# Optimization experiments

Hardware: AMD Instinct MI355X
Metric: run time of the kernel (lower is better)

Reference implementation:

```python
import jax, jax.numpy as jnp
import numpy as np
from jax.scipy.special import gammaln

TEMP = 1.0
PRIOR = 0.2
THRESHOLD = 0.5
EPS = 1e-12


def _normalize(x):
    # F.normalize: x / max(||x||_2, eps)
    n = jnp.linalg.norm(x, axis=-1, keepdims=True)
    return x / jnp.maximum(n, EPS)


def setup_inputs() -> dict:
    key = jax.random.key(0)
    k1, k2 = jax.random.split(key, 2)
    B, L, D = 8, 4096, 512
    hidden = jax.random.normal(k1, (B, L, D), dtype=jnp.float32)
    # uniform noise for RelaxedBernoulli rsample (probs shape is (B, L) after left-pad)
    noise = jax.random.uniform(k2, (B, L), dtype=jnp.float32, minval=1e-6, maxval=1.0 - 1e-6)
    # learned projections, initialized to identity as in the module
    q_w = jnp.eye(D, dtype=jnp.float32)
    k_w = jnp.eye(D, dtype=jnp.float32)
    return {"hidden": hidden, "q_w": q_w, "k_w": k_w, "noise": noise}


def reference(hidden, q_w, k_w, noise):
    B, L, D = hidden.shape
    # cosine-similarity boundary scoring between adjacent tokens
    q = _normalize(hidden[:, :-1]) @ q_w.T  # (B, L-1, D)
    k = _normalize(hidden[:, 1:]) @ k_w.T   # (B, L-1, D)
    cos_sim = jnp.einsum('bld,bld->bl', q, k)  # (B, L-1)
    probs = jnp.clip((1.0 - cos_sim) / 2.0, 0.0, 1.0)
    probs = jnp.pad(probs, ((0, 0), (1, 0)), constant_values=1.0)  # (B, L), first pos always boundary

    # RelaxedBernoulli rsample: sigmoid((logits + logistic_noise) / temp)
    logits = jnp.log(probs) - jnp.log1p(-probs)
    lnoise = jnp.log(noise) - jnp.log1p(-noise)
    soft_boundaries = jax.nn.sigmoid((logits + lnoise) / TEMP)

    # straight-through hard threshold
    hard_f = (soft_boundaries > THRESHOLD).astype(soft_boundaries.dtype)
    hard_boundaries = hard_f - jax.lax.stop_gradient(soft_boundaries) + soft_boundaries

    # dynamic segment pooling (`delete`): segment id = cumsum(boundaries) - 1,
    # mean-pool tokens of each segment; output padded to L segments.
    seg = jnp.clip(jnp.cumsum(hard_boundaries, axis=1).astype(jnp.int32) - 1, 0, L - 1)  # (B, L)

    def pool_one(h, s):
        sums = jax.ops.segment_sum(h, s, num_segments=L)                       # (L, D)
        cnts = jax.ops.segment_sum(jnp.ones((h.shape[0],), h.dtype), s, num_segments=L)
        return sums / jnp.maximum(cnts, 1.0)[:, None]

    pooled = jax.vmap(pool_one)(hidden, seg)   # (B, L, D) (empty segments are zeros)
    pooled = pooled.transpose(1, 0, 2)          # (L, B, D) per `.transpose(0, 1)`

    # Binomial(n=L, p=prior) log-prob loss on number of boundaries per row
    n = jnp.asarray(L, dtype=hidden.dtype)
    ksum = hard_boundaries.sum(axis=-1)  # (B,)
    log_prob = (gammaln(n + 1.0) - gammaln(ksum + 1.0) - gammaln(n - ksum + 1.0)
                + ksum * jnp.log(jnp.asarray(PRIOR, hidden.dtype))
                + (n - ksum) * jnp.log1p(-jnp.asarray(PRIOR, hidden.dtype)))
    loss = -jnp.mean(log_prob) / n
    return pooled, loss
```

## Files before the change

### kernel.cpp

```cpp
#include <hip/hip_runtime.h>
#include <hip/hip_bf16.h>
#include <math.h>

#define B_ 8
#define L_ 4096
#define D_ 512
#define STRIP 8

typedef float f4 __attribute__((ext_vector_type(4)));


__device__ __forceinline__ float wave_reduce_add(float v) {
#pragma unroll
    for (int o = 32; o > 0; o >>= 1) v += __shfl_xor(v, o, 64);
    return v;
}

__global__ __launch_bounds__(256) void k_check(const float* __restrict__ q_w,
                                               const float* __restrict__ k_w,
                                               int* __restrict__ nonid_arr) {
    int t = blockIdx.x * 256 + threadIdx.x;
    bool bad = false;
    for (int i4 = t; i4 < (D_ * D_) / 4; i4 += 64 * 256) {
        int flat = i4 * 4;
        int r = flat >> 9, c0 = flat & (D_ - 1);
        f4 q = *(const f4*)(q_w + flat);
        f4 k = *(const f4*)(k_w + flat);
        float ev[4] = {0.f, 0.f, 0.f, 0.f};
        int dj = r - c0;
        if (dj >= 0 && dj < 4) ev[dj] = 1.0f;
        bad |= (q.x != ev[0]) || (q.y != ev[1]) || (q.z != ev[2]) || (q.w != ev[3]);
        bad |= (k.x != ev[0]) || (k.y != ev[1]) || (k.z != ev[2]) || (k.w != ev[3]);
    }
    unsigned long long m = __ballot(bad);
    __shared__ unsigned long long s[4];
    if ((threadIdx.x & 63) == 0) s[threadIdx.x >> 6] = m;
    __syncthreads();
    if (threadIdx.x == 0)
        nonid_arr[blockIdx.x] = ((s[0] | s[1] | s[2] | s[3]) != 0ull) ? 1 : 0;
}

__global__ __launch_bounds__(256, 4) void k_dotdec(const float* __restrict__ hidden,
                                                   const float* __restrict__ noise,
                                                   const float* __restrict__ q_w,
                                                   const float* __restrict__ k_w,
                                                   const int* __restrict__ nonid_arr,
                                                   unsigned long long* __restrict__ hard64) {
    __shared__ float lds[4 * 2 * D_];
    int wid = threadIdx.x >> 6;
    int lane = threadIdx.x & 63;
    int wave = blockIdx.x * 4 + wid;
    int b = wave >> 9;
    int t0 = (wave & 511) * STRIP;
    const float* base = hidden + (size_t)b * L_ * D_;
    bool nonid = __any(nonid_arr[lane] != 0);
    int i0 = lane * 4, i1 = lane * 4 + 256;
    int rp = (t0 > 0) ? (t0 - 1) : 0;

    if (!nonid) {
        f4 A[9], Bv[9];
#pragma unroll
        for (int i = 0; i < 9; ++i) {
            int r = (i == 0) ? rp : (t0 + i - 1);
            const float* rc = base + (size_t)r * D_;
            A[i] = *(const f4*)(rc + i0);
            Bv[i] = *(const f4*)(rc + i1);
        }
        float ss0 = (A[0].x * A[0].x + A[0].y * A[0].y + A[0].z * A[0].z + A[0].w * A[0].w) +
                    (Bv[0].x * Bv[0].x + Bv[0].y * Bv[0].y + Bv[0].z * Bv[0].z + Bv[0].w * Bv[0].w);
        float dp[STRIP], sp[STRIP];
#pragma unroll
        for (int i = 0; i < STRIP; ++i) {
            dp[i] = (A[i].x * A[i + 1].x + A[i].y * A[i + 1].y +
                     A[i].z * A[i + 1].z + A[i].w * A[i + 1].w) +
                    (Bv[i].x * Bv[i + 1].x + Bv[i].y * Bv[i + 1].y +
                     Bv[i].z * Bv[i + 1].z + Bv[i].w * Bv[i + 1].w);
            sp[i] = (A[i + 1].x * A[i + 1].x + A[i + 1].y * A[i + 1].y +
                     A[i + 1].z * A[i + 1].z + A[i + 1].w * A[i + 1].w) +
                    (Bv[i + 1].x * Bv[i + 1].x + Bv[i + 1].y * Bv[i + 1].y +
                     Bv[i + 1].z * Bv[i + 1].z + Bv[i + 1].w * Bv[i + 1].w);
        }
        float ss0r = wave_reduce_add(ss0);
#pragma unroll
        for (int i = 0; i < STRIP; ++i) {
            dp[i] = wave_reduce_add(dp[i]);
            sp[i] = wave_reduce_add(sp[i]);
        }
        float myDp = dp[7], mySsr = sp[7], mySsl = sp[6];
#pragma unroll
        for (int i = 0; i < 7; ++i) {
            if (lane == i) {
                myDp = dp[i];
                mySsr = sp[i];
                mySsl = (i == 0) ? ss0r : sp[i - 1];
            }
        }
        float u = noise[b * L_ + t0 + (lane & 7)];
        float nl = fmaxf(sqrtf(mySsl), 1e-12f);
        float nr = fmaxf(sqrtf(mySsr), 1e-12f);
        float cosv = myDp / (nl * nr);
        float p = fminf(fmaxf(0.5f * (1.0f - cosv), 0.0f), 1.0f);
        float x = (logf(p) - log1pf(-p)) + (logf(u) - log1pf(-u));
        float sg = 1.0f / (1.0f + expf(-x));
        unsigned long long bm = __ballot(sg > 0.5f);
        if (lane == 0) {
            unsigned long long m = 0;
#pragma unroll
            for (int i = 0; i < 8; ++i) m |= ((bm >> i) & 1ull) << (8 * i);
            if (t0 == 0) m = (m & ~0xFFull) | 1ull;
            hard64[wave] = m;
        }
    } else {
        f4 pa = *(const f4*)(base + (size_t)rp * D_ + i0);
        f4 pb = *(const f4*)(base + (size_t)rp * D_ + i1);
        float ssl;
        {
            float s = pa.x * pa.x + pa.y * pa.y + pa.z * pa.z + pa.w * pa.w;
            float s2 = pb.x * pb.x + pb.y * pb.y + pb.z * pb.z + pb.w * pb.w;
            ssl = wave_reduce_add(s + s2);
        }
        unsigned long long mask = 0;
        for (int i = 0; i < STRIP; ++i) {
            int l = t0 + i;
            unsigned char h;
            const float* rc = base + (size_t)l * D_;
            f4 ca = *(const f4*)(rc + i0);
            f4 cb = *(const f4*)(rc + i1);
            float ssr = (ca.x * ca.x + ca.y * ca.y + ca.z * ca.z + ca.w * ca.w) +
                        (cb.x * cb.x + cb.y * cb.y + cb.z * cb.z + cb.w * cb.w);
            ssr = wave_reduce_add(ssr);
            if (l == 0) {
                h = 1;
            } else {
                float nl = fmaxf(sqrtf(ssl), 1e-12f);
                float nr = fmaxf(sqrtf(ssr), 1e-12f);
                float* nL = lds + wid * 2 * D_;
                float* nR = nL + D_;
                nL[i0 + 0] = pa.x / nl; nL[i0 + 1] = pa.y / nl;
                nL[i0 + 2] = pa.z / nl; nL[i0 + 3] = pa.w / nl;
                nL[i1 + 0] = pb.x / nl; nL[i1 + 1] = pb.y / nl;
                nL[i1 + 2] = pb.z / nl; nL[i1 + 3] = pb.w / nl;
                nR[i0 + 0] = ca.x / nr; nR[i0 + 1] = ca.y / nr;
                nR[i0 + 2] = ca.z / nr; nR[i0 + 3] = ca.w / nr;
                nR[i1 + 0] = cb.x / nr; nR[i1 + 1] = cb.y / nr;
                nR[i1 + 2] = cb.z / nr; nR[i1 + 3] = cb.w / nr;
                float acc = 0.f;
                for (int r8 = 0; r8 < 8; ++r8) {
                    int row = lane + 64 * r8;
                    float qi = 0.f, ki = 0.f;
                    for (int j = 0; j < D_; ++j) {
                        qi += q_w[row * D_ + j] * nL[j];
                        ki += k_w[row * D_ + j] * nR[j];
                    }
                    acc += qi * ki;
                }
                float cosv = wave_reduce_add(acc);
                float p = fminf(fmaxf(0.5f * (1.0f - cosv), 0.0f), 1.0f);
                float u = noise[b * L_ + l];
                float x = (logf(p) - log1pf(-p)) + (logf(u) - log1pf(-u));
                float sg = 1.0f / (1.0f + expf(-x));
                h = (sg > 0.5f) ? (unsigned char)1 : (unsigned char)0;
            }
            mask |= ((unsigned long long)h) << (8 * i);
            pa = ca; pb = cb; ssl = ssr;
        }
        if (lane == 0) hard64[wave] = mask;
    }
}

__global__ __launch_bounds__(256) void k_scan(const unsigned char* __restrict__ hard,
                                              int* __restrict__ seg_starts,
                                              int* __restrict__ ksum) {
    int b = blockIdx.x;
    int tid = threadIdx.x;
    int lane = tid & 63, w = tid >> 6;
    const uint4* hb = (const uint4*)(hard + b * L_);
    uint4 v = hb[tid];
    int s = __popc(v.x) + __popc(v.y) + __popc(v.z) + __popc(v.w);
    int incl = s;
#pragma unroll
    for (int off = 1; off < 64; off <<= 1) {
        int t = __shfl_up(incl, off, 64);
        if (lane >= off) incl += t;
    }
    __shared__ int wtot[4];
    if (lane == 63) wtot[w] = incl;
    __syncthreads();
    int woff = 0;
#pragma unroll
    for (int k = 0; k < 4; ++k)
        if (k < w) woff += wtot[k];
    int run = woff + incl - s;
    int base = tid * 16;
    unsigned wds[4] = {v.x, v.y, v.z, v.w};
#pragma unroll
    for (int wi = 0; wi < 4; ++wi)
#pragma unroll
        for (int byte = 0; byte < 4; ++byte)
            if ((wds[wi] >> (8 * byte)) & 1) {
                run++;
                seg_starts[b * L_ + run - 1] = base + wi * 4 + byte;
            }
    if (tid == 255) ksum[b] = woff + incl;
}

__global__ __launch_bounds__(256) void k_pool(const float* __restrict__ hidden,
                                              const int* __restrict__ seg_starts,
                                              const int* __restrict__ ksum,
                                              float* __restrict__ out,
                                              float* __restrict__ out_loss) {
    int wid = threadIdx.x >> 6, lane = threadIdx.x & 63;
    int j = blockIdx.x * 4 + wid, b = blockIdx.y;
    int S = ksum[b];
    int i0 = lane * 4, i1 = i0 + 256;
    f4 a0 = (f4)(0.0f);
    f4 a1 = (f4)(0.0f);
    if (j < S) {
        int start = seg_starts[b * L_ + j];
        int end = (j + 1 < S) ? seg_starts[b * L_ + j + 1] : L_;
        const float* base = hidden + ((size_t)b * L_ + start) * D_;
        for (int t = start; t < end; ++t, base += D_) {
            f4 v0 = *(const f4*)(base + i0);
            f4 v1 = *(const f4*)(base + i1);
            a0 += v0;
            a1 += v1;
        }
        float len = (float)(end - start);
        a0.x /= len; a0.y /= len; a0.z /= len; a0.w /= len;
        a1.x /= len; a1.y /= len; a1.z /= len; a1.w /= len;
    }
    float* o = out + ((size_t)j * B_ + b) * D_;
    __builtin_nontemporal_store(a0, (f4*)(o + i0));
    __builtin_nontemporal_store(a1, (f4*)(o + i1));

    if (blockIdx.x == gridDim.x - 1 && blockIdx.y == 0) {
        __shared__ double sh[17];
        int tid = threadIdx.x;
        double n = (double)L_;
        if (tid < 8) sh[tid] = lgamma((double)ksum[tid] + 1.0);
        else if (tid < 16) sh[tid] = lgamma(n - (double)ksum[tid - 8] + 1.0);
        else if (tid == 16) sh[16] = lgamma(n + 1.0);
        __syncthreads();
        if (tid == 0) {
            double acc = 0.0, lg = sh[16];
            for (int bb = 0; bb < 8; ++bb) {
                double k = (double)ksum[bb];
                acc += lg - sh[bb] - sh[8 + bb] + k * log(0.2) + (n - k) * log(0.8);
            }
            out_loss[0] = (float)(-(acc / 8.0) / n);
        }
    }
}

extern "C" void kernel_launch(void* const* d_in, const int* in_sizes, int n_in,
                              void* d_out, int out_size, void* d_ws, size_t ws_size,
                              hipStream_t stream) {
    const float* hidden = (const float*)d_in[0];
    const float* q_w = (const float*)d_in[1];
    const float* k_w = (const float*)d_in[2];
    const float* noise = (const float*)d_in[3];
    float* out = (float*)d_out;

    char* ws = (char*)d_ws;
    int* nonid_arr = (int*)(ws + 0);
    int* ksum = (int*)(ws + 512);
    unsigned char* hard = (unsigned char*)(ws + 1024);
    unsigned long long* hard64 = (unsigned long long*)(ws + 1024);
    int* seg_starts = (int*)(ws + 34816);

    k_check<<<64, 256, 0, stream>>>(q_w, k_w, nonid_arr);
    k_dotdec<<<(B_ * L_ / STRIP) / 4, 256, 0, stream>>>(hidden, noise, q_w, k_w,
                                                        nonid_arr, hard64);
    k_scan<<<B_, 256, 0, stream>>>(hard, seg_starts, ksum);
    k_pool<<<dim3(L_ / 4, B_), 256, 0, stream>>>(hidden, seg_starts, ksum, out,
                                                 out + (size_t)L_ * B_ * D_);
}
```

Before: 49.39 us.

## Fuse check, boundary, scan and pool stages into one cooperative persistent kernel

Merges the four separate launches into a single cooperative kernel that uses grid-wide syncs between the identity check, boundary decision, per-batch scan and segment pooling stages. Work is distributed with persistent grid-stride loops over waves, and pooling now processes 8 segments per wave. The aim is to remove inter-kernel launch gaps and tail effects. The cost is grid-sync overhead, and the scan stage runs on only 8 blocks while the rest of the grid waits. A fallback to the multi-kernel path is kept if the cooperative launch fails.

```diff
diff --git a/kernel.cpp b/kernel.cpp
--- a/kernel.cpp
+++ b/kernel.cpp
@@ -1,4 +1,5 @@
 #include <hip/hip_runtime.h>
+#include <hip/hip_cooperative_groups.h>
 #include <hip/hip_bf16.h>
 #include <math.h>
 
@@ -6,8 +7,12 @@
 #define L_ 4096
 #define D_ 512
 #define STRIP 8
+#define GRID_WANT 1024
+#define NWAVE (B_ * L_ / STRIP)
 
 typedef float f4 __attribute__((ext_vector_type(4)));
+
+namespace cg = cooperative_groups;
 
 
 __device__ __forceinline__ float wave_reduce_add(float v) {
@@ -16,44 +21,16 @@
     return v;
 }
 
-__global__ __launch_bounds__(256) void k_check(const float* __restrict__ q_w,
-                                               const float* __restrict__ k_w,
-                                               int* __restrict__ nonid_arr) {
-    int t = blockIdx.x * 256 + threadIdx.x;
-    bool bad = false;
-    for (int i4 = t; i4 < (D_ * D_) / 4; i4 += 64 * 256) {
-        int flat = i4 * 4;
-        int r = flat >> 9, c0 = flat & (D_ - 1);
-        f4 q = *(const f4*)(q_w + flat);
-        f4 k = *(const f4*)(k_w + flat);
-        float ev[4] = {0.f, 0.f, 0.f, 0.f};
-        int dj = r - c0;
-        if (dj >= 0 && dj < 4) ev[dj] = 1.0f;
-        bad |= (q.x != ev[0]) || (q.y != ev[1]) || (q.z != ev[2]) || (q.w != ev[3]);
-        bad |= (k.x != ev[0]) || (k.y != ev[1]) || (k.z != ev[2]) || (k.w != ev[3]);
-    }
-    unsigned long long m = __ballot(bad);
-    __shared__ unsigned long long s[4];
-    if ((threadIdx.x & 63) == 0) s[threadIdx.x >> 6] = m;
-    __syncthreads();
-    if (threadIdx.x == 0)
-        nonid_arr[blockIdx.x] = ((s[0] | s[1] | s[2] | s[3]) != 0ull) ? 1 : 0;
-}
-
-__global__ __launch_bounds__(256, 4) void k_dotdec(const float* __restrict__ hidden,
-                                                   const float* __restrict__ noise,
-                                                   const float* __restrict__ q_w,
-                                                   const float* __restrict__ k_w,
-                                                   const int* __restrict__ nonid_arr,
-                                                   unsigned long long* __restrict__ hard64) {
-    __shared__ float lds[4 * 2 * D_];
-    int wid = threadIdx.x >> 6;
-    int lane = threadIdx.x & 63;
-    int wave = blockIdx.x * 4 + wid;
+
+__device__ __forceinline__ void boundary_wave(int wave, const float* __restrict__ hidden,
+                                              const float* __restrict__ noise,
+                                              const float* __restrict__ q_w,
+                                              const float* __restrict__ k_w,
+                                              bool nonid, float* lds_wave, int lane,
+                                              unsigned long long* hard64) {
     int b = wave >> 9;
     int t0 = (wave & 511) * STRIP;
     const float* base = hidden + (size_t)b * L_ * D_;
-    bool nonid = __any(nonid_arr[lane] != 0);
     int i0 = lane * 4, i1 = lane * 4 + 256;
     int rp = (t0 > 0) ? (t0 - 1) : 0;
 
@@ -134,7 +111,7 @@
             } else {
                 float nl = fmaxf(sqrtf(ssl), 1e-12f);
                 float nr = fmaxf(sqrtf(ssr), 1e-12f);
-                float* nL = lds + wid * 2 * D_;
+                float* nL = lds_wave;
                 float* nR = nL + D_;
                 nL[i0 + 0] = pa.x / nl; nL[i0 + 1] = pa.y / nl;
                 nL[i0 + 2] = pa.z / nl; nL[i0 + 3] = pa.w / nl;
@@ -168,6 +145,174 @@
     }
 }
 
+__device__ __forceinline__ void pool_wave(int wave, const float* __restrict__ hidden,
+                                          const int* __restrict__ seg_starts,
+                                          const int* __restrict__ ksum, int lane,
+                                          float* __restrict__ out) {
+    int b = wave & 7;
+    int jbase = (wave >> 3) * 8;
+    int S = ksum[b];
+    int i0 = lane * 4, i1 = i0 + 256;
+    for (int k = 0; k < 8; ++k) {
+        int j = jbase + k;
+        f4 a0 = (f4)(0.0f);
+        f4 a1 = (f4)(0.0f);
+        if (j < S) {
+            int start = seg_starts[b * L_ + j];
+            int end = (j + 1 < S) ? seg_starts[b * L_ + j + 1] : L_;
+            const float* base = hidden + ((size_t)b * L_ + start) * D_;
+            for (int t = start; t < end; ++t, base += D_) {
+                a0 += *(const f4*)(base + i0);
+                a1 += *(const f4*)(base + i1);
+            }
+            float len = (float)(end - start);
+            a0.x /= len; a0.y /= len; a0.z /= len; a0.w /= len;
+            a1.x /= len; a1.y /= len; a1.z /= len; a1.w /= len;
+        }
+        float* o = out + ((size_t)j * B_ + b) * D_;
+        __builtin_nontemporal_store(a0, (f4*)(o + i0));
+        __builtin_nontemporal_store(a1, (f4*)(o + i1));
+    }
+}
+
+__global__ __launch_bounds__(256, 4) void k_fused(
+    const float* __restrict__ hidden, const float* __restrict__ noise,
+    const float* __restrict__ q_w, const float* __restrict__ k_w,
+    int* __restrict__ nonid_arr, int* __restrict__ ksum,
+    unsigned long long* hard64_arg,
+    int* __restrict__ seg_starts, float* __restrict__ out,
+    float* __restrict__ out_loss) {
+    cg::grid_group grid = cg::this_grid();
+    unsigned long long* hard64 = hard64_arg;
+    const unsigned char* hard = (const unsigned char*)hard64_arg;
+    int bid = blockIdx.x, tid = threadIdx.x;
+    int wid = tid >> 6, lane = tid & 63;
+    int nb = gridDim.x;
+
+    __shared__ float lds[4 * 2 * D_];
+    __shared__ unsigned long long sb[4];
+    __shared__ int wtot[4];
+    __shared__ double sh[17];
+
+    for (int c = bid; c < 256; c += nb) {
+        int flat = (c * 256 + tid) * 4;
+        int r = flat >> 9, c0 = flat & (D_ - 1);
+        f4 q = *(const f4*)(q_w + flat);
+        f4 k = *(const f4*)(k_w + flat);
+        float ev[4] = {0.f, 0.f, 0.f, 0.f};
+        int dj = r - c0;
+        if (dj >= 0 && dj < 4) ev[dj] = 1.0f;
+        bool bad = (q.x != ev[0]) || (q.y != ev[1]) || (q.z != ev[2]) || (q.w != ev[3]) ||
+                   (k.x != ev[0]) || (k.y != ev[1]) || (k.z != ev[2]) || (k.w != ev[3]);
+        unsigned long long m = __ballot(bad);
+        if (lane == 0) sb[wid] = m;
+        __syncthreads();
+        if (tid == 0)
+            nonid_arr[c] = ((sb[0] | sb[1] | sb[2] | sb[3]) != 0ull) ? 1 : 0;
+        __syncthreads();
+    }
+    grid.sync();
+
+    {
+        int4 nf = ((const int4*)nonid_arr)[lane];
+        bool nonid = __any((nf.x | nf.y | nf.z | nf.w) != 0);
+        for (int wave = bid * 4 + wid; wave < NWAVE; wave += nb * 4)
+            boundary_wave(wave, hidden, noise, q_w, k_w, nonid,
+                          lds + wid * 2 * D_, lane, hard64);
+    }
+    grid.sync();
+
+    if (bid < B_) {
+        int b = bid;
+        const uint4* hb = (const uint4*)(hard + b * L_);
+        uint4 v = hb[tid];
+        int s = __popc(v.x) + __popc(v.y) + __popc(v.z) + __popc(v.w);
+        int incl = s;
+#pragma unroll
+        for (int off = 1; off < 64; off <<= 1) {
+            int t = __shfl_up(incl, off, 64);
+            if (lane >= off) incl += t;
+        }
+        if (lane == 63) wtot[wid] = incl;
+        __syncthreads();
+        int woff = 0;
+#pragma unroll
+        for (int k = 0; k < 4; ++k)
+            if (k < wid) woff += wtot[k];
+        int run = woff + incl - s;
+        int base = tid * 16;
+        unsigned wds[4] = {v.x, v.y, v.z, v.w};
+#pragma unroll
+        for (int wi = 0; wi < 4; ++wi)
+#pragma unroll
+            for (int byte = 0; byte < 4; ++byte)
+                if ((wds[wi] >> (8 * byte)) & 1) {
+                    run++;
+                    seg_starts[b * L_ + run - 1] = base + wi * 4 + byte;
+                }
+        if (tid == 255) ksum[b] = woff + incl;
+    }
+    grid.sync();
+
+    for (int wave = bid * 4 + wid; wave < NWAVE; wave += nb * 4)
+        pool_wave(wave, hidden, seg_starts, ksum, lane, out);
+
+    if (bid == 0) {
+        double n = (double)L_;
+        if (tid < 8) sh[tid] = lgamma((double)ksum[tid] + 1.0);
+        else if (tid < 16) sh[tid] = lgamma(n - (double)ksum[tid - 8] + 1.0);
+        else if (tid == 16) sh[16] = lgamma(n + 1.0);
+        __syncthreads();
+        if (tid == 0) {
+            double acc = 0.0, lg = sh[16];
+            for (int bb = 0; bb < 8; ++bb) {
+                double k = (double)ksum[bb];
+                acc += lg - sh[bb] - sh[8 + bb] + k * log(0.2) + (n - k) * log(0.8);
+            }
+            out_loss[0] = (float)(-(acc / 8.0) / n);
+        }
+    }
+}
+
+__global__ __launch_bounds__(256) void k_check(const float* __restrict__ q_w,
+                                               const float* __restrict__ k_w,
+                                               int* __restrict__ nonid_arr) {
+    int t = blockIdx.x * 256 + threadIdx.x;
+    bool bad = false;
+    for (int i4 = t; i4 < (D_ * D_) / 4; i4 += 64 * 256) {
+        int flat = i4 * 4;
+        int r = flat >> 9, c0 = flat & (D_ - 1);
+        f4 q = *(const f4*)(q_w + flat);
+        f4 k = *(const f4*)(k_w + flat);
+        float ev[4] = {0.f, 0.f, 0.f, 0.f};
+        int dj = r - c0;
+        if (dj >= 0 && dj < 4) ev[dj] = 1.0f;
+        bad |= (q.x != ev[0]) || (q.y != ev[1]) || (q.z != ev[2]) || (q.w != ev[3]);
+        bad |= (k.x != ev[0]) || (k.y != ev[1]) || (k.z != ev[2]) || (k.w != ev[3]);
+    }
+    unsigned long long m = __ballot(bad);
+    __shared__ unsigned long long s[4];
+    if ((threadIdx.x & 63) == 0) s[threadIdx.x >> 6] = m;
+    __syncthreads();
+    if (threadIdx.x == 0)
+        nonid_arr[blockIdx.x] = ((s[0] | s[1] | s[2] | s[3]) != 0ull) ? 1 : 0;
+}
+
+__global__ __launch_bounds__(256, 4) void k_dotdec(const float* __restrict__ hidden,
+                                                   const float* __restrict__ noise,
+                                                   const float* __restrict__ q_w,
+                                                   const float* __restrict__ k_w,
+                                                   const int* __restrict__ nonid_arr,
+                                                   unsigned long long* __restrict__ hard64) {
+    __shared__ float lds[4 * 2 * D_];
+    int wid = threadIdx.x >> 6;
+    int lane = threadIdx.x & 63;
+    int wave = blockIdx.x * 4 + wid;
+    bool nonid = __any(nonid_arr[lane] != 0);
+    boundary_wave(wave, hidden, noise, q_w, k_w, nonid, lds + wid * 2 * D_, lane,
+                  hard64);
+}
+
 __global__ __launch_bounds__(256) void k_scan(const unsigned char* __restrict__ hard,
                                               int* __restrict__ seg_starts,
                                               int* __restrict__ ksum) {
@@ -210,30 +355,10 @@
                                               float* __restrict__ out,
                                               float* __restrict__ out_loss) {
     int wid = threadIdx.x >> 6, lane = threadIdx.x & 63;
-    int j = blockIdx.x * 4 + wid, b = blockIdx.y;
-    int S = ksum[b];
-    int i0 = lane * 4, i1 = i0 + 256;
-    f4 a0 = (f4)(0.0f);
-    f4 a1 = (f4)(0.0f);
-    if (j < S) {
-        int start = seg_starts[b * L_ + j];
-        int end = (j + 1 < S) ? seg_starts[b * L_ + j + 1] : L_;
-        const float* base = hidden + ((size_t)b * L_ + start) * D_;
-        for (int t = start; t < end; ++t, base += D_) {
-            f4 v0 = *(const f4*)(base + i0);
-            f4 v1 = *(const f4*)(base + i1);
-            a0 += v0;
-            a1 += v1;
-        }
-        float len = (float)(end - start);
-        a0.x /= len; a0.y /= len; a0.z /= len; a0.w /= len;
-        a1.x /= len; a1.y /= len; a1.z /= len; a1.w /= len;
-    }
-    float* o = out + ((size_t)j * B_ + b) * D_;
-    __builtin_nontemporal_store(a0, (f4*)(o + i0));
-    __builtin_nontemporal_store(a1, (f4*)(o + i1));
-
-    if (blockIdx.x == gridDim.x - 1 && blockIdx.y == 0) {
+    int wave = blockIdx.x * 4 + wid;
+    pool_wave(wave, hidden, seg_starts, ksum, lane, out);
+
+    if (blockIdx.x == gridDim.x - 1) {
         __shared__ double sh[17];
         int tid = threadIdx.x;
         double n = (double)L_;
@@ -260,18 +385,38 @@
     const float* k_w = (const float*)d_in[2];
     const float* noise = (const float*)d_in[3];
     float* out = (float*)d_out;
+    float* out_loss = out + (size_t)L_ * B_ * D_;
 
     char* ws = (char*)d_ws;
     int* nonid_arr = (int*)(ws + 0);
-    int* ksum = (int*)(ws + 512);
-    unsigned char* hard = (unsigned char*)(ws + 1024);
-    unsigned long long* hard64 = (unsigned long long*)(ws + 1024);
+    int* ksum = (int*)(ws + 1024);
+    unsigned char* hard = (unsigned char*)(ws + 2048);
+    unsigned long long* hard64 = (unsigned long long*)(ws + 2048);
     int* seg_starts = (int*)(ws + 34816);
 
-    k_check<<<64, 256, 0, stream>>>(q_w, k_w, nonid_arr);
-    k_dotdec<<<(B_ * L_ / STRIP) / 4, 256, 0, stream>>>(hidden, noise, q_w, k_w,
-                                                        nonid_arr, hard64);
-    k_scan<<<B_, 256, 0, stream>>>(hard, seg_starts, ksum);
-    k_pool<<<dim3(L_ / 4, B_), 256, 0, stream>>>(hidden, seg_starts, ksum, out,
-                                                 out + (size_t)L_ * B_ * D_);
-}
+    int numCU = 0, maxPerCU = 0;
+    int dev = 0;
+    bool coop_ok = (hipGetDevice(&dev) == hipSuccess) &&
+                   (hipDeviceGetAttribute(&numCU, hipDeviceAttributeMultiprocessorCount,
+                                          dev) == hipSuccess) &&
+                   (hipOccupancyMaxActiveBlocksPerMultiprocessor(&maxPerCU, k_fused, 256,
+                                                                 0) == hipSuccess) &&
+                   (maxPerCU >= 1) && (numCU * maxPerCU >= 8);
+    if (coop_ok) {
+        int G = numCU * maxPerCU;
+        if (G > GRID_WANT) G = GRID_WANT;
+        void* args[] = {(void*)&hidden, (void*)&noise, (void*)&q_w, (void*)&k_w,
+                        (void*)&nonid_arr, (void*)&ksum, (void*)&hard64,
+                        (void*)&seg_starts, (void*)&out, (void*)&out_loss};
+        coop_ok = (hipLaunchCooperativeKernel((void*)k_fused, dim3(G), dim3(256), args,
+                                              0, stream) == hipSuccess);
+    }
+    if (!coop_ok) {
+        k_check<<<64, 256, 0, stream>>>(q_w, k_w, nonid_arr);
+        k_dotdec<<<NWAVE / 4, 256, 0, stream>>>(hidden, noise, q_w, k_w, nonid_arr,
+                                                hard64);
+        k_scan<<<B_, 256, 0, stream>>>(hard, seg_starts, ksum);
+        k_pool<<<NWAVE / 4 / 8, 256, 0, stream>>>(hidden, seg_starts, ksum, out,
+                                                  out_loss);
+    }
+}
```

Result: slower. 189.8 us (+284.2%).

## Fuse identity check into dot kernel, split fixup path, merge scan with pooling

Applied to the files above, without the earlier changes.

Moves the q_w/k_w identity check into the main adjacency-dot kernel, so each of the 1024 blocks checks 256 weight elements. The general projection path moves to a separate fixup kernel that exits early when the weights are identity. The scan and pooling kernels merge into one: each block recomputes the row's segment starts into LDS and pools 32 segments, and the loss block recomputes per-row boundary counts. This cuts kernel launches and global seg_starts traffic, at the cost of a redundant scan in every pooling block and an extra fixup launch.

```diff
diff --git a/kernel.cpp b/kernel.cpp
--- a/kernel.cpp
+++ b/kernel.cpp
@@ -6,6 +6,7 @@
 #define L_ 4096
 #define D_ 512
 #define STRIP 8
+#define NWAVE (B_ * L_ / STRIP)
 
 typedef float f4 __attribute__((ext_vector_type(4)));
 
@@ -16,166 +17,184 @@
     return v;
 }
 
-__global__ __launch_bounds__(256) void k_check(const float* __restrict__ q_w,
-                                               const float* __restrict__ k_w,
-                                               int* __restrict__ nonid_arr) {
-    int t = blockIdx.x * 256 + threadIdx.x;
-    bool bad = false;
-    for (int i4 = t; i4 < (D_ * D_) / 4; i4 += 64 * 256) {
-        int flat = i4 * 4;
-        int r = flat >> 9, c0 = flat & (D_ - 1);
-        f4 q = *(const f4*)(q_w + flat);
-        f4 k = *(const f4*)(k_w + flat);
-        float ev[4] = {0.f, 0.f, 0.f, 0.f};
-        int dj = r - c0;
-        if (dj >= 0 && dj < 4) ev[dj] = 1.0f;
-        bad |= (q.x != ev[0]) || (q.y != ev[1]) || (q.z != ev[2]) || (q.w != ev[3]);
-        bad |= (k.x != ev[0]) || (k.y != ev[1]) || (k.z != ev[2]) || (k.w != ev[3]);
-    }
-    unsigned long long m = __ballot(bad);
-    __shared__ unsigned long long s[4];
-    if ((threadIdx.x & 63) == 0) s[threadIdx.x >> 6] = m;
+__device__ __forceinline__ int wave_reduce_add_i(int v) {
+#pragma unroll
+    for (int o = 32; o > 0; o >>= 1) v += __shfl_xor(v, o, 64);
+    return v;
+}
+
+__global__ __launch_bounds__(256, 4) void k_main(const float* __restrict__ hidden,
+                                                 const float* __restrict__ noise,
+                                                 const float* __restrict__ q_w,
+                                                 const float* __restrict__ k_w,
+                                                 int* __restrict__ nonid_arr,
+                                                 unsigned long long* __restrict__ hard64) {
+    int bid = blockIdx.x, tid = threadIdx.x;
+    int wid = tid >> 6, lane = tid & 63;
+
+    {
+        int i = bid * 256 + tid;
+        int r = i >> 9, c = i & (D_ - 1);
+        float e = (r == c) ? 1.0f : 0.0f;
+        bool bad = (q_w[i] != e) || (k_w[i] != e);
+        unsigned long long m = __ballot(bad);
+        __shared__ unsigned long long sb[4];
+        if (lane == 0) sb[wid] = m;
+        __syncthreads();
+        if (tid == 0)
+            nonid_arr[bid] = ((sb[0] | sb[1] | sb[2] | sb[3]) != 0ull) ? 1 : 0;
+    }
+
+    int wave = bid * 4 + wid;
+    int b = wave >> 9;
+    int t0 = (wave & 511) * STRIP;
+    const float* base = hidden + (size_t)b * L_ * D_;
+    int i0 = lane * 4, i1 = lane * 4 + 256;
+    int rp = (t0 > 0) ? (t0 - 1) : 0;
+
+    f4 A[9], Bv[9];
+#pragma unroll
+    for (int i = 0; i < 9; ++i) {
+        int r = (i == 0) ? rp : (t0 + i - 1);
+        const float* rc = base + (size_t)r * D_;
+        A[i] = *(const f4*)(rc + i0);
+        Bv[i] = *(const f4*)(rc + i1);
+    }
+    float ss0 = (A[0].x * A[0].x + A[0].y * A[0].y + A[0].z * A[0].z + A[0].w * A[0].w) +
+                (Bv[0].x * Bv[0].x + Bv[0].y * Bv[0].y + Bv[0].z * Bv[0].z + Bv[0].w * Bv[0].w);
+    float dp[STRIP], sp[STRIP];
+#pragma unroll
+    for (int i = 0; i < STRIP; ++i) {
+        dp[i] = (A[i].x * A[i + 1].x + A[i].y * A[i + 1].y +
+                 A[i].z * A[i + 1].z + A[i].w * A[i + 1].w) +
+                (Bv[i].x * Bv[i + 1].x + Bv[i].y * Bv[i + 1].y +
+                 Bv[i].z * Bv[i + 1].z + Bv[i].w * Bv[i + 1].w);
+        sp[i] = (A[i + 1].x * A[i + 1].x + A[i + 1].y * A[i + 1].y +
+                 A[i + 1].z * A[i + 1].z + A[i + 1].w * A[i + 1].w) +
+                (Bv[i + 1].x * Bv[i + 1].x + Bv[i + 1].y * Bv[i + 1].y +
+                 Bv[i + 1].z * Bv[i + 1].z + Bv[i + 1].w * Bv[i + 1].w);
+    }
+    float ss0r = wave_reduce_add(ss0);
+#pragma unroll
+    for (int i = 0; i < STRIP; ++i) {
+        dp[i] = wave_reduce_add(dp[i]);
+        sp[i] = wave_reduce_add(sp[i]);
+    }
+    float myDp = dp[7], mySsr = sp[7], mySsl = sp[6];
+#pragma unroll
+    for (int i = 0; i < 7; ++i) {
+        if (lane == i) {
+            myDp = dp[i];
+            mySsr = sp[i];
+            mySsl = (i == 0) ? ss0r : sp[i - 1];
+        }
+    }
+    float u = noise[b * L_ + t0 + (lane & 7)];
+    float nl = fmaxf(sqrtf(mySsl), 1e-12f);
+    float nr = fmaxf(sqrtf(mySsr), 1e-12f);
+    float cosv = myDp / (nl * nr);
+    float p = fminf(fmaxf(0.5f * (1.0f - cosv), 0.0f), 1.0f);
+    float x = (logf(p) - log1pf(-p)) + (logf(u) - log1pf(-u));
+    float sg = 1.0f / (1.0f + expf(-x));
+    unsigned long long bm = __ballot(sg > 0.5f);
+    if (lane == 0) {
+        unsigned long long m = 0;
+#pragma unroll
+        for (int i = 0; i < 8; ++i) m |= ((bm >> i) & 1ull) << (8 * i);
+        if (t0 == 0) m = (m & ~0xFFull) | 1ull;
+        hard64[wave] = m;
+    }
+}
+
+__global__ __launch_bounds__(256, 2) void k_fixup(const float* __restrict__ hidden,
+                                                  const float* __restrict__ noise,
+                                                  const float* __restrict__ q_w,
+                                                  const float* __restrict__ k_w,
+                                                  const int* __restrict__ nonid_arr,
+                                                  unsigned long long* __restrict__ hard64) {
+    __shared__ float lds[4 * 2 * D_];
+    __shared__ int sbad[4];
+    int tid = threadIdx.x, wid = tid >> 6, lane = tid & 63;
+    int4 nf = ((const int4*)nonid_arr)[tid];
+    bool bad = __any((nf.x | nf.y | nf.z | nf.w) != 0);
+    if (lane == 0) sbad[wid] = bad ? 1 : 0;
     __syncthreads();
-    if (threadIdx.x == 0)
-        nonid_arr[blockIdx.x] = ((s[0] | s[1] | s[2] | s[3]) != 0ull) ? 1 : 0;
-}
-
-__global__ __launch_bounds__(256, 4) void k_dotdec(const float* __restrict__ hidden,
-                                                   const float* __restrict__ noise,
-                                                   const float* __restrict__ q_w,
-                                                   const float* __restrict__ k_w,
-                                                   const int* __restrict__ nonid_arr,
-                                                   unsigned long long* __restrict__ hard64) {
-    __shared__ float lds[4 * 2 * D_];
-    int wid = threadIdx.x >> 6;
-    int lane = threadIdx.x & 63;
+    if ((sbad[0] | sbad[1] | sbad[2] | sbad[3]) == 0) return;
+
     int wave = blockIdx.x * 4 + wid;
     int b = wave >> 9;
     int t0 = (wave & 511) * STRIP;
     const float* base = hidden + (size_t)b * L_ * D_;
-    bool nonid = __any(nonid_arr[lane] != 0);
     int i0 = lane * 4, i1 = lane * 4 + 256;
     int rp = (t0 > 0) ? (t0 - 1) : 0;
 
-    if (!nonid) {
-        f4 A[9], Bv[9];
-#pragma unroll
-        for (int i = 0; i < 9; ++i) {
-            int r = (i == 0) ? rp : (t0 + i - 1);
-            const float* rc = base + (size_t)r * D_;
-            A[i] = *(const f4*)(rc + i0);
-            Bv[i] = *(const f4*)(rc + i1);
-        }
-        float ss0 = (A[0].x * A[0].x + A[0].y * A[0].y + A[0].z * A[0].z + A[0].w * A[0].w) +
-                    (Bv[0].x * Bv[0].x + Bv[0].y * Bv[0].y + Bv[0].z * Bv[0].z + Bv[0].w * Bv[0].w);
-        float dp[STRIP], sp[STRIP];
-#pragma unroll
-        for (int i = 0; i < STRIP; ++i) {
-            dp[i] = (A[i].x * A[i + 1].x + A[i].y * A[i + 1].y +
-                     A[i].z * A[i + 1].z + A[i].w * A[i + 1].w) +
-                    (Bv[i].x * Bv[i + 1].x + Bv[i].y * Bv[i + 1].y +
-                     Bv[i].z * Bv[i + 1].z + Bv[i].w * Bv[i + 1].w);
-            sp[i] = (A[i + 1].x * A[i + 1].x + A[i + 1].y * A[i + 1].y +
-                     A[i + 1].z * A[i + 1].z + A[i + 1].w * A[i + 1].w) +
-                    (Bv[i + 1].x * Bv[i + 1].x + Bv[i + 1].y * Bv[i + 1].y +
-                     Bv[i + 1].z * Bv[i + 1].z + Bv[i + 1].w * Bv[i + 1].w);
-        }
-        float ss0r = wave_reduce_add(ss0);
-#pragma unroll
-        for (int i = 0; i < STRIP; ++i) {
-            dp[i] = wave_reduce_add(dp[i]);
-            sp[i] = wave_reduce_add(sp[i]);
-        }
-        float myDp = dp[7], mySsr = sp[7], mySsl = sp[6];
-#pragma unroll
-        for (int i = 0; i < 7; ++i) {
-            if (lane == i) {
-                myDp = dp[i];
-                mySsr = sp[i];
-                mySsl = (i == 0) ? ss0r : sp[i - 1];
-            }
-        }
-        float u = noise[b * L_ + t0 + (lane & 7)];
-        float nl = fmaxf(sqrtf(mySsl), 1e-12f);
-        float nr = fmaxf(sqrtf(mySsr), 1e-12f);
-        float cosv = myDp / (nl * nr);
-        float p = fminf(fmaxf(0.5f * (1.0f - cosv), 0.0f), 1.0f);
-        float x = (logf(p) - log1pf(-p)) + (logf(u) - log1pf(-u));
-        float sg = 1.0f / (1.0f + expf(-x));
-        unsigned long long bm = __ballot(sg > 0.5f);
-        if (lane == 0) {
-            unsigned long long m = 0;
-#pragma unroll
-            for (int i = 0; i < 8; ++i) m |= ((bm >> i) & 1ull) << (8 * i);
-            if (t0 == 0) m = (m & ~0xFFull) | 1ull;
-            hard64[wave] = m;
-        }
-    } else {
-        f4 pa = *(const f4*)(base + (size_t)rp * D_ + i0);
-        f4 pb = *(const f4*)(base + (size_t)rp * D_ + i1);
-        float ssl;
-        {
-            float s = pa.x * pa.x + pa.y * pa.y + pa.z * pa.z + pa.w * pa.w;
-            float s2 = pb.x * pb.x + pb.y * pb.y + pb.z * pb.z + pb.w * pb.w;
-            ssl = wave_reduce_add(s + s2);
-        }
-        unsigned long long mask = 0;
-        for (int i = 0; i < STRIP; ++i) {
-            int l = t0 + i;
-            unsigned char h;
-            const float* rc = base + (size_t)l * D_;
-            f4 ca = *(const f4*)(rc + i0);
-            f4 cb = *(const f4*)(rc + i1);
-            float ssr = (ca.x * ca.x + ca.y * ca.y + ca.z * ca.z + ca.w * ca.w) +
-                        (cb.x * cb.x + cb.y * cb.y + cb.z * cb.z + cb.w * cb.w);
-            ssr = wave_reduce_add(ssr);
-            if (l == 0) {
-                h = 1;
-            } else {
-                float nl = fmaxf(sqrtf(ssl), 1e-12f);
-                float nr = fmaxf(sqrtf(ssr), 1e-12f);
-                float* nL = lds + wid * 2 * D_;
-                float* nR = nL + D_;
-                nL[i0 + 0] = pa.x / nl; nL[i0 + 1] = pa.y / nl;
-                nL[i0 + 2] = pa.z / nl; nL[i0 + 3] = pa.w / nl;
-                nL[i1 + 0] = pb.x / nl; nL[i1 + 1] = pb.y / nl;
-                nL[i1 + 2] = pb.z / nl; nL[i1 + 3] = pb.w / nl;
-                nR[i0 + 0] = ca.x / nr; nR[i0 + 1] = ca.y / nr;
-                nR[i0 + 2] = ca.z / nr; nR[i0 + 3] = ca.w / nr;
-                nR[i1 + 0] = cb.x / nr; nR[i1 + 1] = cb.y / nr;
-                nR[i1 + 2] = cb.z / nr; nR[i1 + 3] = cb.w / nr;
-                float acc = 0.f;
-                for (int r8 = 0; r8 < 8; ++r8) {
-                    int row = lane + 64 * r8;
-                    float qi = 0.f, ki = 0.f;
-                    for (int j = 0; j < D_; ++j) {
-                        qi += q_w[row * D_ + j] * nL[j];
-                        ki += k_w[row * D_ + j] * nR[j];
-                    }
-                    acc += qi * ki;
+    f4 pa = *(const f4*)(base + (size_t)rp * D_ + i0);
+    f4 pb = *(const f4*)(base + (size_t)rp * D_ + i1);
+    float ssl;
+    {
+        float s = pa.x * pa.x + pa.y * pa.y + pa.z * pa.z + pa.w * pa.w;
+        float s2 = pb.x * pb.x + pb.y * pb.y + pb.z * pb.z + pb.w * pb.w;
+        ssl = wave_reduce_add(s + s2);
+    }
+    unsigned long long mask = 0;
+    for (int i = 0; i < STRIP; ++i) {
+        int l = t0 + i;
+        unsigned char h;
+        const float* rc = base + (size_t)l * D_;
+        f4 ca = *(const f4*)(rc + i0);
+        f4 cb = *(const f4*)(rc + i1);
+        float ssr = (ca.x * ca.x + ca.y * ca.y + ca.z * ca.z + ca.w * ca.w) +
+                    (cb.x * cb.x + cb.y * cb.y + cb.z * cb.z + cb.w * cb.w);
+        ssr = wave_reduce_add(ssr);
+        if (l == 0) {
+            h = 1;
+        } else {
+            float nl = fmaxf(sqrtf(ssl), 1e-12f);
+            float nr = fmaxf(sqrtf(ssr), 1e-12f);
+            float* nL = lds + wid * 2 * D_;
+            float* nR = nL + D_;
+            nL[i0 + 0] = pa.x / nl; nL[i0 + 1] = pa.y / nl;
+            nL[i0 + 2] = pa.z / nl; nL[i0 + 3] = pa.w / nl;
+            nL[i1 + 0] = pb.x / nl; nL[i1 + 1] = pb.y / nl;
+            nL[i1 + 2] = pb.z / nl; nL[i1 + 3] = pb.w / nl;
+            nR[i0 + 0] = ca.x / nr; nR[i0 + 1] = ca.y / nr;
+            nR[i0 + 2] = ca.z / nr; nR[i0 + 3] = ca.w / nr;
+            nR[i1 + 0] = cb.x / nr; nR[i1 + 1] = cb.y / nr;
+            nR[i1 + 2] = cb.z / nr; nR[i1 + 3] = cb.w / nr;
+            float acc = 0.f;
+            for (int r8 = 0; r8 < 8; ++r8) {
+                int row = lane + 64 * r8;
+                float qi = 0.f, ki = 0.f;
+                for (int j = 0; j < D_; ++j) {
+                    qi += q_w[row * D_ + j] * nL[j];
+                    ki += k_w[row * D_ + j] * nR[j];
                 }
-                float cosv = wave_reduce_add(acc);
-                float p = fminf(fmaxf(0.5f * (1.0f - cosv), 0.0f), 1.0f);
-                float u = noise[b * L_ + l];
-                float x = (logf(p) - log1pf(-p)) + (logf(u) - log1pf(-u));
-                float sg = 1.0f / (1.0f + expf(-x));
-                h = (sg > 0.5f) ? (unsigned char)1 : (unsigned char)0;
-            }
-            mask |= ((unsigned long long)h) << (8 * i);
-            pa = ca; pb = cb; ssl = ssr;
-        }
-        if (lane == 0) hard64[wave] = mask;
-    }
-}
-
-__global__ __launch_bounds__(256) void k_scan(const unsigned char* __restrict__ hard,
-                                              int* __restrict__ seg_starts,
-                                              int* __restrict__ ksum) {
-    int b = blockIdx.x;
-    int tid = threadIdx.x;
-    int lane = tid & 63, w = tid >> 6;
-    const uint4* hb = (const uint4*)(hard + b * L_);
-    uint4 v = hb[tid];
+                acc += qi * ki;
+            }
+            float cosv = wave_reduce_add(acc);
+            float p = fminf(fmaxf(0.5f * (1.0f - cosv), 0.0f), 1.0f);
+            float u = noise[b * L_ + l];
+            float x = (logf(p) - log1pf(-p)) + (logf(u) - log1pf(-u));
+            float sg = 1.0f / (1.0f + expf(-x));
+            h = (sg > 0.5f) ? (unsigned char)1 : (unsigned char)0;
+        }
+        mask |= ((unsigned long long)h) << (8 * i);
+        pa = ca; pb = cb; ssl = ssr;
+    }
+    if (lane == 0) hard64[wave] = mask;
+}
+
+__global__ __launch_bounds__(256) void k_scanpool(const float* __restrict__ hidden,
+                                                  const unsigned char* __restrict__ hard,
+                                                  float* __restrict__ out,
+                                                  float* __restrict__ out_loss) {
+    int bx = blockIdx.x, b = blockIdx.y;
+    int tid = threadIdx.x, wid = tid >> 6, lane = tid & 63;
+    __shared__ int seg_lds[L_];
+    __shared__ int wtot[4];
+    __shared__ int s_S;
+
+    uint4 v = ((const uint4*)(hard + b * L_))[tid];
     int s = __popc(v.x) + __popc(v.y) + __popc(v.z) + __popc(v.w);
     int incl = s;
 #pragma unroll
@@ -183,15 +202,14 @@
         int t = __shfl_up(incl, off, 64);
         if (lane >= off) incl += t;
     }
-    __shared__ int wtot[4];
-    if (lane == 63) wtot[w] = incl;
+    if (lane == 63) wtot[wid] = incl;
     __syncthreads();
     int woff = 0;
 #pragma unroll
     for (int k = 0; k < 4; ++k)
-        if (k < w) woff += wtot[k];
+        if (k < wid) woff += wtot[k];
     int run = woff + incl - s;
-    int base = tid * 16;
+    int pbase = tid * 16;
     unsigned wds[4] = {v.x, v.y, v.z, v.w};
 #pragma unroll
     for (int wi = 0; wi < 4; ++wi)
@@ -199,52 +217,57 @@
         for (int byte = 0; byte < 4; ++byte)
             if ((wds[wi] >> (8 * byte)) & 1) {
                 run++;
-                seg_starts[b * L_ + run - 1] = base + wi * 4 + byte;
-            }
-    if (tid == 255) ksum[b] = woff + incl;
-}
-
-__global__ __launch_bounds__(256) void k_pool(const float* __restrict__ hidden,
-                                              const int* __restrict__ seg_starts,
-                                              const int* __restrict__ ksum,
-                                              float* __restrict__ out,
-                                              float* __restrict__ out_loss) {
-    int wid = threadIdx.x >> 6, lane = threadIdx.x & 63;
-    int j = blockIdx.x * 4 + wid, b = blockIdx.y;
-    int S = ksum[b];
+                seg_lds[run - 1] = pbase + wi * 4 + byte;
+            }
+    if (tid == 255) s_S = woff + incl;
+    __syncthreads();
+    int S = s_S;
+
     int i0 = lane * 4, i1 = i0 + 256;
-    f4 a0 = (f4)(0.0f);
-    f4 a1 = (f4)(0.0f);
-    if (j < S) {
-        int start = seg_starts[b * L_ + j];
-        int end = (j + 1 < S) ? seg_starts[b * L_ + j + 1] : L_;
-        const float* base = hidden + ((size_t)b * L_ + start) * D_;
-        for (int t = start; t < end; ++t, base += D_) {
-            f4 v0 = *(const f4*)(base + i0);
-            f4 v1 = *(const f4*)(base + i1);
-            a0 += v0;
-            a1 += v1;
-        }
-        float len = (float)(end - start);
-        a0.x /= len; a0.y /= len; a0.z /= len; a0.w /= len;
-        a1.x /= len; a1.y /= len; a1.z /= len; a1.w /= len;
-    }
-    float* o = out + ((size_t)j * B_ + b) * D_;
-    __builtin_nontemporal_store(a0, (f4*)(o + i0));
-    __builtin_nontemporal_store(a1, (f4*)(o + i1));
-
-    if (blockIdx.x == gridDim.x - 1 && blockIdx.y == 0) {
+    int jbase = bx * 32 + wid * 8;
+    for (int k = 0; k < 8; ++k) {
+        int j = jbase + k;
+        f4 a0 = (f4)(0.0f);
+        f4 a1 = (f4)(0.0f);
+        if (j < S) {
+            int start = seg_lds[j];
+            int end = (j + 1 < S) ? seg_lds[j + 1] : L_;
+            const float* base = hidden + ((size_t)b * L_ + start) * D_;
+            for (int t = start; t < end; ++t, base += D_) {
+                a0 += *(const f4*)(base + i0);
+                a1 += *(const f4*)(base + i1);
+            }
+            float len = (float)(end - start);
+            a0.x /= len; a0.y /= len; a0.z /= len; a0.w /= len;
+            a1.x /= len; a1.y /= len; a1.z /= len; a1.w /= len;
+        }
+        float* o = out + ((size_t)j * B_ + b) * D_;
+        __builtin_nontemporal_store(a0, (f4*)(o + i0));
+        __builtin_nontemporal_store(a1, (f4*)(o + i1));
+    }
+
+    if (bx == 0 && b == 0) {
+        __shared__ int ksum_lds[8];
+        __shared__ int wsum[4];
         __shared__ double sh[17];
-        int tid = threadIdx.x;
+        for (int bb = 0; bb < 8; ++bb) {
+            uint4 vv = ((const uint4*)(hard + bb * L_))[tid];
+            int ss = __popc(vv.x) + __popc(vv.y) + __popc(vv.z) + __popc(vv.w);
+            ss = wave_reduce_add_i(ss);
+            if (lane == 0) wsum[wid] = ss;
+            __syncthreads();
+            if (tid == 0) ksum_lds[bb] = wsum[0] + wsum[1] + wsum[2] + wsum[3];
+            __syncthreads();
+        }
         double n = (double)L_;
-        if (tid < 8) sh[tid] = lgamma((double)ksum[tid] + 1.0);
-        else if (tid < 16) sh[tid] = lgamma(n - (double)ksum[tid - 8] + 1.0);
+        if (tid < 8) sh[tid] = lgamma((double)ksum_lds[tid] + 1.0);
+        else if (tid < 16) sh[tid] = lgamma(n - (double)ksum_lds[tid - 8] + 1.0);
         else if (tid == 16) sh[16] = lgamma(n + 1.0);
         __syncthreads();
         if (tid == 0) {
             double acc = 0.0, lg = sh[16];
             for (int bb = 0; bb < 8; ++bb) {
-                double k = (double)ksum[bb];
+                double k = (double)ksum_lds[bb];
                 acc += lg - sh[bb] - sh[8 + bb] + k * log(0.2) + (n - k) * log(0.8);
             }
             out_loss[0] = (float)(-(acc / 8.0) / n);
@@ -260,18 +283,14 @@
     const float* k_w = (const float*)d_in[2];
     const float* noise = (const float*)d_in[3];
     float* out = (float*)d_out;
+    float* out_loss = out + (size_t)L_ * B_ * D_;
 
     char* ws = (char*)d_ws;
     int* nonid_arr = (int*)(ws + 0);
-    int* ksum = (int*)(ws + 512);
-    unsigned char* hard = (unsigned char*)(ws + 1024);
-    unsigned long long* hard64 = (unsigned long long*)(ws + 1024);
-    int* seg_starts = (int*)(ws + 34816);
-
-    k_check<<<64, 256, 0, stream>>>(q_w, k_w, nonid_arr);
-    k_dotdec<<<(B_ * L_ / STRIP) / 4, 256, 0, stream>>>(hidden, noise, q_w, k_w,
-                                                        nonid_arr, hard64);
-    k_scan<<<B_, 256, 0, stream>>>(hard, seg_starts, ksum);
-    k_pool<<<dim3(L_ / 4, B_), 256, 0, stream>>>(hidden, seg_starts, ksum, out,
-                                                 out + (size_t)L_ * B_ * D_);
-}
+    unsigned long long* hard64 = (unsigned long long*)(ws + 4096);
+    unsigned char* hard = (unsigned char*)(ws + 4096);
+
+    k_main<<<NWAVE / 4, 256, 0, stream>>>(hidden, noise, q_w, k_w, nonid_arr, hard64);
+    k_fixup<<<NWAVE / 4, 256, 0, stream>>>(hidden, noise, q_w, k_w, nonid_arr, hard64);
+    k_scanpool<<<dim3(L_ / 32, B_), 256, 0, stream>>>(hidden, hard, out, out_loss);
+}
```

After: 47.64 us. -3.5%, faster.
